# Optimization experiments

Measured on AMD Instinct MI355X. Metric: run time of the kernel, lower is better.

## Reference

```python
import jax, jax.numpy as jnp
import numpy as np

EMB = 1024
NHEAD = 16
DILATIONS = (1, 4, 8, 16)
KSIZE = 7
ROT_DIM = 32  # RotaryEmbedding(dim=32): only first 32 channels of each head rotated


def neighbor_idx(T, k, d):
    # NATTEN-style 1D dilated neighborhood: window of k positions on the
    # dilation lattice (same residue class mod d), centered and clamped at borders.
    i = jnp.arange(T)
    r = i % d                      # residue class
    p = i // d                     # position within class
    Lr = (T - r + d - 1) // d      # class length
    s = jnp.clip(p - k // 2, 0, Lr - k)
    j = jnp.arange(k)
    return r[:, None] + (s[:, None] + j[None, :]) * d  # [T, k] int indices


def rope(x, rot_dim=ROT_DIM):
    # lucidrains RotaryEmbedding.rotate_queries_or_keys: interleaved pairs,
    # applied over seq dim (-2), only first rot_dim channels.
    T = x.shape[-2]
    inv = 1.0 / (10000.0 ** (jnp.arange(0, rot_dim, 2, dtype=jnp.float32) / rot_dim))
    freqs = jnp.arange(T, dtype=jnp.float32)[:, None] * inv[None, :]  # [T, rot_dim//2]
    freqs = jnp.repeat(freqs, 2, axis=-1)                             # [T, rot_dim]
    cos, sin = jnp.cos(freqs), jnp.sin(freqs)
    xr, xp = x[..., :rot_dim], x[..., rot_dim:]
    x1, x2 = xr[..., 0::2], xr[..., 1::2]
    rot = jnp.stack([-x2, x1], axis=-1).reshape(xr.shape)
    return jnp.concatenate([xr * cos + rot * sin, xp], axis=-1)


def setup_inputs() -> dict:
    key = jax.random.key(0)
    ks = jax.random.split(key, 5)
    B, T, C = 4, 8192, EMB
    s = 0.02
    return {
        "x": jax.random.normal(ks[0], (B, T, C), jnp.float32),
        "wq": jax.random.normal(ks[1], (C, C), jnp.float32) * s,
        "bq": jnp.zeros((C,), jnp.float32),
        "wk": jax.random.normal(ks[2], (C, C), jnp.float32) * s,
        "bk": jnp.zeros((C,), jnp.float32),
        "wv": jax.random.normal(ks[3], (C, C), jnp.float32) * s,
        "bv": jnp.zeros((C,), jnp.float32),
        "wp": jax.random.normal(ks[4], (C, C), jnp.float32) * s,
        "bp": jnp.zeros((C,), jnp.float32),
    }


def reference(x, wq, bq, wk, bk, wv, bv, wp, bp):
    B, T, C = x.shape
    hs = C // NHEAD

    def heads(w, b):  # torch Linear: x @ W^T + b, then [B, nh, T, hs]
        return (x @ w.T + b).reshape(B, T, NHEAD, hs).transpose(0, 2, 1, 3)

    q, k, v = heads(wq, bq), heads(wk, bk), heads(wv, bv)
    present = jnp.stack([k, v])  # pre-rotary kv cache, as in original

    q, k, v = rope(q), rope(k), rope(v)  # original also rotates v

    gsz = NHEAD // len(DILATIONS)
    outs = []
    for gi, d in enumerate(DILATIONS):
        sl = slice(gi * gsz, (gi + 1) * gsz)
        idx = neighbor_idx(T, KSIZE, d)           # [T, K]
        kk = k[:, sl][:, :, idx]                   # [B, g, T, K, hs]
        vv = v[:, sl][:, :, idx]                   # [B, g, T, K, hs]
        scores = jnp.einsum('bgtd,bgtkd->bgtk', q[:, sl], kk)  # no 1/sqrt(hs), as na1d_qk
        attn = jax.nn.softmax(scores, axis=-1)
        outs.append(jnp.einsum('bgtk,bgtkd->bgtd', attn, vv))
    y = jnp.concatenate(outs, axis=1)              # [B, nh, T, hs]
    y = y.transpose(0, 2, 1, 3).reshape(B, T, C)
    y = y @ wp.T + bp
    return (y, present)
```

## Files before the change

kernel.cpp:

```cpp
#include <hip/hip_runtime.h>

typedef unsigned short ushortT;
typedef unsigned int uint32;
typedef __attribute__((ext_vector_type(8))) short short8;
typedef __attribute__((ext_vector_type(4))) float f32x4;

__device__ __forceinline__ ushortT f2bf(float f) {
    uint32 u = __float_as_uint(f);
    uint32 r = (u + 0x7fffu + ((u >> 16) & 1u)) >> 16;
    return (ushortT)r;
}
__device__ __forceinline__ float bf2f(uint32 v) {
    return __uint_as_float(v << 16);
}

__device__ __forceinline__ void unpack8(uint4 v, float* f) {
    f[0] = bf2f(v.x & 0xffffu); f[1] = bf2f(v.x >> 16);
    f[2] = bf2f(v.y & 0xffffu); f[3] = bf2f(v.y >> 16);
    f[4] = bf2f(v.z & 0xffffu); f[5] = bf2f(v.z >> 16);
    f[6] = bf2f(v.w & 0xffffu); f[7] = bf2f(v.w >> 16);
}

typedef __attribute__((address_space(1))) const void gvoid;
typedef __attribute__((address_space(3))) void lvoid;
__device__ __forceinline__ void gld16(const ushortT* g, ushortT* l) {
    __builtin_amdgcn_global_load_lds((gvoid*)g, (lvoid*)l, 16, 0, 0);
}

__global__ __launch_bounds__(256) void f32_to_bf16_kernel(
    const float* __restrict__ src, ushortT* __restrict__ dst, int n4)
{
    int i = blockIdx.x * 256 + threadIdx.x;
    if (i < n4) {
        float4 v = reinterpret_cast<const float4*>(src)[i];
        ushort4 o;
        o.x = f2bf(v.x); o.y = f2bf(v.y); o.z = f2bf(v.z); o.w = f2bf(v.w);
        reinterpret_cast<ushort4*>(dst)[i] = o;
    }
}

__global__ __launch_bounds__(256) void wconv_kernel(
    const float* __restrict__ s0, const float* __restrict__ s1,
    const float* __restrict__ s2, const float* __restrict__ s3,
    ushortT* __restrict__ dst)
{
    int i = blockIdx.x * 256 + threadIdx.x;
    const int wsel = i >> 18;
    const int off  = i & 262143;
    const float* s = (wsel == 0) ? s0 : (wsel == 1 ? s1 : (wsel == 2 ? s2 : s3));
    float4 v = reinterpret_cast<const float4*>(s)[off];
    ushort4 o;
    o.x = f2bf(v.x); o.y = f2bf(v.y); o.z = f2bf(v.z); o.w = f2bf(v.w);
    reinterpret_cast<ushort4*>(dst)[i] = o;
}

__global__ __launch_bounds__(256) void pack_bias_kernel(
    const float* __restrict__ bq, const float* __restrict__ bk,
    const float* __restrict__ bv, float* __restrict__ out)
{
    int i = blockIdx.x * 256 + threadIdx.x;
    float v = (i < 1024) ? bq[i] : (i < 2048 ? bk[i - 1024] : bv[i - 2048]);
    out[i] = v;
}

__global__ __launch_bounds__(256) void rope_table_kernel(float2* __restrict__ tab)
{
    int idx = blockIdx.x * 256 + threadIdx.x;
    int t = idx >> 4;
    int i = idx & 15;
    float inv = powf(10000.0f, -(float)i / 16.0f);
    float ang = (float)t * inv;
    tab[idx] = make_float2(cosf(ang), sinf(ang));
}


__device__ __forceinline__ short8 ldsfrag(const ushortT* region, int row, int g) {
    int e = (row << 5) + (g << 3);
    e ^= ((row >> 1) & 3) << 3;
    return *reinterpret_cast<const short8*>(region + e);
}

#define MC_ ((size_t)33554432)

template<int MODE>
__global__ __launch_bounds__(512, 2) void gemm256_kernel(
    const ushortT* __restrict__ A,
    const ushortT* __restrict__ Wall,
    const float*   __restrict__ biasAll,
    const float2*  __restrict__ tab,
    ushortT*       __restrict__ CbAll,
    float*         __restrict__ CfAll,
    int M, int N, int K)
{
    extern __shared__ ushortT lds[];
    const int tid  = threadIdx.x;
    const int lane = tid & 63;
    const int wv   = tid >> 6;
    const int wm   = wv >> 2;
    const int wn   = wv & 3;
    const int g    = lane >> 4;
    const int rsel = lane & 15;

    const int bidAll = blockIdx.x;
    const int proj   = (MODE == 3) ? (bidAll >> 9) : 0;
    const int bid    = (MODE == 3) ? (bidAll & 511) : bidAll;

    const ushortT* W    = Wall + (size_t)proj * 1024 * K;
    const float*   bias = biasAll + proj * 1024;

    const int xi  = bid & 7;
    const int j   = bid >> 3;
    const int tn  = j & 3;
    const int tm  = xi * 16 + (j >> 2);
    const int m0  = tm * 256, n0 = tn * 256;

    const int crow = tid >> 2;
    const int ccol = ((tid & 3) ^ ((tid >> 3) & 3)) * 8;
    const ushortT* gA0 = A + (size_t)(m0 + crow) * K + ccol;
    const ushortT* gA1 = gA0 + (size_t)128 * K;
    const ushortT* gB0 = W + (size_t)(n0 + crow) * K + ccol;
    const ushortT* gB1 = gB0 + (size_t)128 * K;

    const int dst0 = wv * 512;
    const int dst1 = 4096 + wv * 512;

    #pragma unroll
    for (int t = 0; t < 3; ++t) {
        ushortT* ra = lds + t * 16384;
        ushortT* rb = ra + 8192;
        gld16(gA0 + t * 32, ra + dst0);
        gld16(gA1 + t * 32, ra + dst1);
        gld16(gB0 + t * 32, rb + dst0);
        gld16(gB1 + t * 32, rb + dst1);
    }
    asm volatile("s_waitcnt vmcnt(8)" ::: "memory");
    __builtin_amdgcn_s_barrier();

    f32x4 acc[8][4] = {};
    const int NT = K >> 5;

    #pragma unroll 1
    for (int t = 0; t < NT; ++t) {
        const ushortT* ra = lds + (t & 3) * 16384;
        const ushortT* rb = ra + 8192;

        short8 Bf[4], Af[4];
        #pragma unroll
        for (int fn = 0; fn < 4; ++fn) Bf[fn] = ldsfrag(rb, wn * 64 + fn * 16 + rsel, g);
        #pragma unroll
        for (int fm = 0; fm < 4; ++fm) Af[fm] = ldsfrag(ra, wm * 128 + fm * 16 + rsel, g);
        if (t + 3 < NT) {
            ushortT* wa = lds + ((t + 3) & 3) * 16384;
            gld16(gA0 + (t + 3) * 32, wa + dst0);
            gld16(gA1 + (t + 3) * 32, wa + dst1);
        }
        asm volatile("" ::: "memory");
        __builtin_amdgcn_s_barrier();
        asm volatile("s_waitcnt lgkmcnt(0)" ::: "memory");
        __builtin_amdgcn_sched_barrier(0);
        __builtin_amdgcn_s_setprio(1);
        #pragma unroll
        for (int fm = 0; fm < 4; ++fm)
            #pragma unroll
            for (int fn = 0; fn < 4; ++fn)
                acc[fm][fn] = __builtin_amdgcn_mfma_f32_16x16x32_bf16(Af[fm], Bf[fn], acc[fm][fn], 0, 0, 0);
        __builtin_amdgcn_s_setprio(0);
        asm volatile("" ::: "memory");
        __builtin_amdgcn_s_barrier();

        #pragma unroll
        for (int fm = 0; fm < 4; ++fm) Af[fm] = ldsfrag(ra, wm * 128 + 64 + fm * 16 + rsel, g);
        if (t + 3 < NT) {
            ushortT* wb = lds + ((t + 3) & 3) * 16384 + 8192;
            gld16(gB0 + (t + 3) * 32, wb + dst0);
            gld16(gB1 + (t + 3) * 32, wb + dst1);
        }
        if (t < NT - 3)      { asm volatile("s_waitcnt vmcnt(8)" ::: "memory"); }
        else if (t == NT - 3){ asm volatile("s_waitcnt vmcnt(4)" ::: "memory"); }
        else if (t == NT - 2){ asm volatile("s_waitcnt vmcnt(0)" ::: "memory"); }
        asm volatile("" ::: "memory");
        __builtin_amdgcn_s_barrier();
        asm volatile("s_waitcnt lgkmcnt(0)" ::: "memory");
        __builtin_amdgcn_sched_barrier(0);
        __builtin_amdgcn_s_setprio(1);
        #pragma unroll
        for (int fm = 0; fm < 4; ++fm)
            #pragma unroll
            for (int fn = 0; fn < 4; ++fn)
                acc[4 + fm][fn] = __builtin_amdgcn_mfma_f32_16x16x32_bf16(Af[fm], Bf[fn], acc[4 + fm][fn], 0, 0, 0);
        __builtin_amdgcn_s_setprio(0);
        asm volatile("" ::: "memory");
        __builtin_amdgcn_s_barrier();
    }

    #pragma unroll
    for (int fn = 0; fn < 4; ++fn) {
        const int colb = n0 + wn * 64 + fn * 16 + rsel;
        const int d    = colb & 63;
        const float bv = bias[colb];
        #pragma unroll
        for (int am = 0; am < 8; ++am) {
            const int rowbase = m0 + wm * 128 + am * 16 + g * 4;
            #pragma unroll
            for (int e = 0; e < 4; ++e) {
                const int row = rowbase + e;
                const float val = acc[am][fn][e] + bv;
                if (MODE == 2) {
                    CfAll[(size_t)row * N + colb] = val;
                } else {
                    if (proj != 0) {
                        const int b = row >> 13, t = row & 8191;
                        const int h = colb >> 6;
                        CfAll[(size_t)(proj - 1) * MC_ +
                              (((size_t)b * 16 + h) * 8192 + t) * 64 + d] = val;
                    }
                    const float pv = __shfl_xor(val, 1, 64);
                    float ov = val;
                    if (d < 32) {
                        const int t = row & 8191;
                        const float2 cs = tab[t * 16 + (d >> 1)];
                        ov = (d & 1) ? fmaf(val, cs.x,  pv * cs.y)
                                     : fmaf(val, cs.x, -pv * cs.y);
                    }
                    CbAll[(size_t)proj * MC_ + (size_t)row * 1024 + colb] = f2bf(ov);
                }
            }
        }
    }
}

__global__ __launch_bounds__(256) void natt_kernel(
    const ushortT* __restrict__ Q,
    const ushortT* __restrict__ Kl,
    const ushortT* __restrict__ Vl,
    ushortT*       __restrict__ O)
{
    const int T = 8192;
    const int tid  = threadIdx.x;
    const int lane = tid & 63;
    const int tloc = lane >> 3;
    const int c    = lane & 7;

    const int wq   = (blockIdx.x * 256 + tid) >> 6;
    const int qidx = wq * 8 + tloc;
    const int t = qidx & (T - 1);
    const int h = (qidx >> 13) & 15;
    const int b = qidx >> 17;

    const int shifts[4] = {0, 2, 3, 4};
    const int sh = shifts[h >> 2];
    const int dd = 1 << sh;

    const int r  = t & (dd - 1);
    const int p  = t >> sh;
    const int Lr = ((T - 1 - r) >> sh) + 1;
    int s = p - 3;
    const int smax = Lr - 7;
    s = s < 0 ? 0 : (s > smax ? smax : s);
    const int tbase = r + (s << sh);

    const size_t qoff = ((size_t)(b * T + t)) * 1024 + h * 64 + c * 8;
    float qf[8];
    unpack8(*reinterpret_cast<const uint4*>(Q + qoff), qf);

    const size_t cbase = ((size_t)b * T) * 1024 + h * 64 + c * 8;

    float sc[7];
    #pragma unroll
    for (int j = 0; j < 7; ++j) {
        const int tj = tbase + (j << sh);
        float kf[8];
        unpack8(*reinterpret_cast<const uint4*>(Kl + cbase + (size_t)tj * 1024), kf);
        float pp = 0.f;
        #pragma unroll
        for (int i = 0; i < 8; ++i) pp = fmaf(qf[i], kf[i], pp);
        pp += __shfl_xor(pp, 1, 64);
        pp += __shfl_xor(pp, 2, 64);
        pp += __shfl_xor(pp, 4, 64);
        sc[j] = pp;
    }

    float mx = sc[0];
    #pragma unroll
    for (int j = 1; j < 7; ++j) mx = fmaxf(mx, sc[j]);
    float den = 0.f;
    #pragma unroll
    for (int j = 0; j < 7; ++j) { sc[j] = __expf(sc[j] - mx); den += sc[j]; }
    const float inv = 1.0f / den;

    float out[8] = {};
    #pragma unroll
    for (int j = 0; j < 7; ++j) {
        const int tj = tbase + (j << sh);
        float vf[8];
        unpack8(*reinterpret_cast<const uint4*>(Vl + cbase + (size_t)tj * 1024), vf);
        #pragma unroll
        for (int i = 0; i < 8; ++i) out[i] = fmaf(sc[j], vf[i], out[i]);
    }

    short8 ov;
    #pragma unroll
    for (int i = 0; i < 8; ++i) ov[i] = (short)f2bf(out[i] * inv);
    *reinterpret_cast<short8*>(const_cast<ushortT*>(O + qoff)) = ov;
}

extern "C" void kernel_launch(void* const* d_in, const int* in_sizes, int n_in,
                              void* d_out, int out_size, void* d_ws, size_t ws_size,
                              hipStream_t stream)
{
    const float* x  = (const float*)d_in[0];
    const float* wq = (const float*)d_in[1];
    const float* bq = (const float*)d_in[2];
    const float* wk = (const float*)d_in[3];
    const float* bk = (const float*)d_in[4];
    const float* wv = (const float*)d_in[5];
    const float* bv = (const float*)d_in[6];
    const float* wp = (const float*)d_in[7];
    const float* bp = (const float*)d_in[8];

    const int B = 4, T = 8192, C = 1024;
    const int M = B * T;
    const size_t MC = (size_t)M * C;

    char* ws = (char*)d_ws;
    ushortT* xb    = (ushortT*)ws;
    ushortT* wallb = (ushortT*)(ws + (size_t)64 * 1024 * 1024);
    ushortT* wpb   = wallb + (size_t)3 * C * C;
    ushortT* qlin  = (ushortT*)(ws + (size_t)72 * 1024 * 1024);
    ushortT* klin  = qlin + MC;
    ushortT* vlin  = klin + MC;
    float2*  tab   = (float2*)(ws + (size_t)264 * 1024 * 1024);
    float*   bqkv  = (float*)(ws + (size_t)266 * 1024 * 1024);

    float* y     = (float*)d_out;
    float* presK = y + MC;

    hipFuncSetAttribute((const void*)gemm256_kernel<3>,
                        hipFuncAttributeMaxDynamicSharedMemorySize, 131072);
    hipFuncSetAttribute((const void*)gemm256_kernel<2>,
                        hipFuncAttributeMaxDynamicSharedMemorySize, 131072);

    rope_table_kernel<<<512, 256, 0, stream>>>(tab);
    pack_bias_kernel<<<12, 256, 0, stream>>>(bq, bk, bv, bqkv);

    f32_to_bf16_kernel<<<(int)(MC / 4 / 256), 256, 0, stream>>>(x, xb, (int)(MC / 4));
    wconv_kernel<<<4 * (C * C / 4) / 256, 256, 0, stream>>>(wq, wk, wv, wp, wallb);

    gemm256_kernel<3><<<1536, 512, 131072, stream>>>(
        xb, wallb, bqkv, tab, qlin, presK, M, C, C);

    natt_kernel<<<(B * 16 * T) / 32, 256, 0, stream>>>(qlin, klin, vlin, xb);

    gemm256_kernel<2><<<512, 512, 131072, stream>>>(
        xb, wpb, bp, tab, nullptr, y, M, C, C);
}
```

Baseline: 591.2 us.

## Replace 256x256 four-stage GEMM with simpler 128x128 double-buffered GEMM

```diff
diff --git a/kernel.cpp b/kernel.cpp
--- a/kernel.cpp
+++ b/kernel.cpp
@@ -83,7 +83,7 @@
 #define MC_ ((size_t)33554432)
 
 template<int MODE>
-__global__ __launch_bounds__(512, 2) void gemm256_kernel(
+__global__ __launch_bounds__(256, 3) void gemm128_kernel(
     const ushortT* __restrict__ A,
     const ushortT* __restrict__ Wall,
     const float*   __restrict__ biasAll,
@@ -92,106 +92,72 @@
     float*         __restrict__ CfAll,
     int M, int N, int K)
 {
-    extern __shared__ ushortT lds[];
+    __shared__ ushortT lds[16384];
     const int tid  = threadIdx.x;
     const int lane = tid & 63;
     const int wv   = tid >> 6;
-    const int wm   = wv >> 2;
-    const int wn   = wv & 3;
+    const int wm   = wv >> 1;
+    const int wn   = wv & 1;
     const int g    = lane >> 4;
     const int rsel = lane & 15;
 
     const int bidAll = blockIdx.x;
-    const int proj   = (MODE == 3) ? (bidAll >> 9) : 0;
-    const int bid    = (MODE == 3) ? (bidAll & 511) : bidAll;
+    const int proj   = (MODE == 3) ? (bidAll >> 11) : 0;
+    const int bid    = (MODE == 3) ? (bidAll & 2047) : bidAll;
 
     const ushortT* W    = Wall + (size_t)proj * 1024 * K;
     const float*   bias = biasAll + proj * 1024;
 
     const int xi  = bid & 7;
     const int j   = bid >> 3;
-    const int tn  = j & 3;
-    const int tm  = xi * 16 + (j >> 2);
-    const int m0  = tm * 256, n0 = tn * 256;
+    const int tn  = j & 7;
+    const int tm  = xi * 32 + (j >> 3);
+    const int m0  = tm * 128, n0 = tn * 128;
 
     const int crow = tid >> 2;
     const int ccol = ((tid & 3) ^ ((tid >> 3) & 3)) * 8;
     const ushortT* gA0 = A + (size_t)(m0 + crow) * K + ccol;
-    const ushortT* gA1 = gA0 + (size_t)128 * K;
+    const ushortT* gA1 = gA0 + (size_t)64 * K;
     const ushortT* gB0 = W + (size_t)(n0 + crow) * K + ccol;
-    const ushortT* gB1 = gB0 + (size_t)128 * K;
+    const ushortT* gB1 = gB0 + (size_t)64 * K;
 
     const int dst0 = wv * 512;
-    const int dst1 = 4096 + wv * 512;
-
-    #pragma unroll
-    for (int t = 0; t < 3; ++t) {
-        ushortT* ra = lds + t * 16384;
-        ushortT* rb = ra + 8192;
-        gld16(gA0 + t * 32, ra + dst0);
-        gld16(gA1 + t * 32, ra + dst1);
-        gld16(gB0 + t * 32, rb + dst0);
-        gld16(gB1 + t * 32, rb + dst1);
-    }
-    asm volatile("s_waitcnt vmcnt(8)" ::: "memory");
-    __builtin_amdgcn_s_barrier();
-
-    f32x4 acc[8][4] = {};
+    const int dst1 = 2048 + wv * 512;
+
+    #define STAGE(buf, t) { \
+        ushortT* base_ = lds + (buf) * 8192; \
+        gld16(gA0 + (t) * 32, base_ + dst0); \
+        gld16(gA1 + (t) * 32, base_ + dst1); \
+        gld16(gB0 + (t) * 32, base_ + 4096 + dst0); \
+        gld16(gB1 + (t) * 32, base_ + 4096 + dst1); \
+    }
+
+    f32x4 acc[4][4] = {};
     const int NT = K >> 5;
+    int cur = 0;
+
+    STAGE(0, 0);
 
     #pragma unroll 1
     for (int t = 0; t < NT; ++t) {
-        const ushortT* ra = lds + (t & 3) * 16384;
-        const ushortT* rb = ra + 8192;
-
-        short8 Bf[4], Af[4];
+        __syncthreads();
+        if (t + 1 < NT) STAGE(cur ^ 1, t + 1);
+
+        const ushortT* ra = lds + cur * 8192;
+        const ushortT* rb = ra + 4096;
+        short8 Af[4], Bf[4];
+        #pragma unroll
+        for (int fm = 0; fm < 4; ++fm) Af[fm] = ldsfrag(ra, wm * 64 + fm * 16 + rsel, g);
         #pragma unroll
         for (int fn = 0; fn < 4; ++fn) Bf[fn] = ldsfrag(rb, wn * 64 + fn * 16 + rsel, g);
-        #pragma unroll
-        for (int fm = 0; fm < 4; ++fm) Af[fm] = ldsfrag(ra, wm * 128 + fm * 16 + rsel, g);
-        if (t + 3 < NT) {
-            ushortT* wa = lds + ((t + 3) & 3) * 16384;
-            gld16(gA0 + (t + 3) * 32, wa + dst0);
-            gld16(gA1 + (t + 3) * 32, wa + dst1);
-        }
-        asm volatile("" ::: "memory");
-        __builtin_amdgcn_s_barrier();
-        asm volatile("s_waitcnt lgkmcnt(0)" ::: "memory");
-        __builtin_amdgcn_sched_barrier(0);
-        __builtin_amdgcn_s_setprio(1);
         #pragma unroll
         for (int fm = 0; fm < 4; ++fm)
             #pragma unroll
             for (int fn = 0; fn < 4; ++fn)
                 acc[fm][fn] = __builtin_amdgcn_mfma_f32_16x16x32_bf16(Af[fm], Bf[fn], acc[fm][fn], 0, 0, 0);
-        __builtin_amdgcn_s_setprio(0);
-        asm volatile("" ::: "memory");
-        __builtin_amdgcn_s_barrier();
-
-        #pragma unroll
-        for (int fm = 0; fm < 4; ++fm) Af[fm] = ldsfrag(ra, wm * 128 + 64 + fm * 16 + rsel, g);
-        if (t + 3 < NT) {
-            ushortT* wb = lds + ((t + 3) & 3) * 16384 + 8192;
-            gld16(gB0 + (t + 3) * 32, wb + dst0);
-            gld16(gB1 + (t + 3) * 32, wb + dst1);
-        }
-        if (t < NT - 3)      { asm volatile("s_waitcnt vmcnt(8)" ::: "memory"); }
-        else if (t == NT - 3){ asm volatile("s_waitcnt vmcnt(4)" ::: "memory"); }
-        else if (t == NT - 2){ asm volatile("s_waitcnt vmcnt(0)" ::: "memory"); }
-        asm volatile("" ::: "memory");
-        __builtin_amdgcn_s_barrier();
-        asm volatile("s_waitcnt lgkmcnt(0)" ::: "memory");
-        __builtin_amdgcn_sched_barrier(0);
-        __builtin_amdgcn_s_setprio(1);
-        #pragma unroll
-        for (int fm = 0; fm < 4; ++fm)
-            #pragma unroll
-            for (int fn = 0; fn < 4; ++fn)
-                acc[4 + fm][fn] = __builtin_amdgcn_mfma_f32_16x16x32_bf16(Af[fm], Bf[fn], acc[4 + fm][fn], 0, 0, 0);
-        __builtin_amdgcn_s_setprio(0);
-        asm volatile("" ::: "memory");
-        __builtin_amdgcn_s_barrier();
-    }
+        cur ^= 1;
+    }
+    #undef STAGE
 
     #pragma unroll
     for (int fn = 0; fn < 4; ++fn) {
@@ -199,12 +165,12 @@
         const int d    = colb & 63;
         const float bv = bias[colb];
         #pragma unroll
-        for (int am = 0; am < 8; ++am) {
-            const int rowbase = m0 + wm * 128 + am * 16 + g * 4;
+        for (int fm = 0; fm < 4; ++fm) {
+            const int rowbase = m0 + wm * 64 + fm * 16 + g * 4;
             #pragma unroll
             for (int e = 0; e < 4; ++e) {
                 const int row = rowbase + e;
-                const float val = acc[am][fn][e] + bv;
+                const float val = acc[fm][fn][e] + bv;
                 if (MODE == 2) {
                     CfAll[(size_t)row * N + colb] = val;
                 } else {
@@ -335,22 +301,17 @@
     float* y     = (float*)d_out;
     float* presK = y + MC;
 
-    hipFuncSetAttribute((const void*)gemm256_kernel<3>,
-                        hipFuncAttributeMaxDynamicSharedMemorySize, 131072);
-    hipFuncSetAttribute((const void*)gemm256_kernel<2>,
-                        hipFuncAttributeMaxDynamicSharedMemorySize, 131072);
-
     rope_table_kernel<<<512, 256, 0, stream>>>(tab);
     pack_bias_kernel<<<12, 256, 0, stream>>>(bq, bk, bv, bqkv);
 
     f32_to_bf16_kernel<<<(int)(MC / 4 / 256), 256, 0, stream>>>(x, xb, (int)(MC / 4));
     wconv_kernel<<<4 * (C * C / 4) / 256, 256, 0, stream>>>(wq, wk, wv, wp, wallb);
 
-    gemm256_kernel<3><<<1536, 512, 131072, stream>>>(
+    gemm128_kernel<3><<<6144, 256, 0, stream>>>(
         xb, wallb, bqkv, tab, qlin, presK, M, C, C);
 
     natt_kernel<<<(B * 16 * T) / 32, 256, 0, stream>>>(qlin, klin, vlin, xb);
 
-    gemm256_kernel<2><<<512, 512, 131072, stream>>>(
+    gemm128_kernel<2><<<2048, 256, 0, stream>>>(
         xb, wpb, bp, tab, nullptr, y, M, C, C);
 }
```

Result: no change. 587.3 us (-0.7%).
